# Optimization experiments

Measured on AMD Instinct MI355X. Metric: run time of the kernel, lower is better.

Reference implementation:

```python
import jax, jax.numpy as jnp
import numpy as np

N_KNN = 16
BN_EPS = 1e-5


def conv1d(x, w, b):
    # x: [B, Cin, N], w: [Cout, Cin], b: [Cout] (1x1 Conv1d)
    return jnp.einsum('oc,bcn->bon', w, x) + b[None, :, None]


def conv2d(x, w, b):
    # x: [B, Cin, N, K], w: [Cout, Cin], b: [Cout] (1x1 Conv2d)
    return jnp.einsum('oc,bcnk->bonk', w, x) + b[None, :, None, None]


def bn2d(x, gamma, beta, mean, var):
    # eval-mode BatchNorm2d over channel axis 1
    scale = (gamma / jnp.sqrt(var + BN_EPS))[None, :, None, None]
    return (x - mean[None, :, None, None]) * scale + beta[None, :, None, None]


def knn_idx(pos, k):
    # pos: [B, 3, N] -> idx: [B, N, K] of k nearest neighbors (incl. self)
    p = jnp.swapaxes(pos, 1, 2)  # [B, N, 3]
    sq = jnp.sum(p * p, axis=-1)  # [B, N]
    d2 = sq[:, :, None] - 2.0 * jnp.einsum('bnd,bmd->bnm', p, p) + sq[:, None, :]
    _, idx = jax.lax.top_k(-d2, k)
    return idx


def group(x, idx):
    # x: [B, C, N], idx: [B, N, K] -> [B, C, N, K] (grouping_operation)
    return jax.vmap(lambda xb, ib: xb[:, ib])(x, idx)


def setup_inputs() -> dict:
    key = jax.random.key(0)
    B, C_OBJ, C_Q, N, DIM, PH, AM = 4, 512, 512, 4096, 128, 64, 4
    ks = jax.random.split(key, 32)
    r = lambda i, sh, s=0.05: jax.random.normal(ks[i], sh, jnp.float32) * s
    inp = {
        'obj_feature': jax.random.normal(ks[0], (B, C_OBJ, N), jnp.float32),
        'pos': jax.random.normal(ks[1], (B, 3, N), jnp.float32),
        'query_points': jax.random.normal(ks[2], (B, C_Q, N), jnp.float32),
        # linear_start_query / linear_start_obj
        'w_sq': r(3, (DIM, C_Q)), 'b_sq': r(4, (DIM,)),
        'w_so': r(5, (DIM, C_OBJ)), 'b_so': r(6, (DIM,)),
        # key / query / value 1x1 convs
        'w_k': r(7, (DIM, DIM)), 'b_k': r(8, (DIM,)),
        'w_q': r(9, (DIM, DIM)), 'b_q': r(10, (DIM,)),
        'w_v': r(11, (DIM, DIM)), 'b_v': r(12, (DIM,)),
        # pos_mlp: Conv2d(3->PH), BN, ReLU, Conv2d(PH->DIM)
        'w_p1': r(13, (PH, 3)), 'b_p1': r(14, (PH,)),
        'g_bn1': 1.0 + r(15, (PH,)), 'be_bn1': r(16, (PH,)),
        'm_bn1': r(17, (PH,)), 'v_bn1': 1.0 + 0.1 * jax.random.uniform(ks[18], (PH,), jnp.float32),
        'w_p2': r(19, (DIM, PH)), 'b_p2': r(20, (DIM,)),
        # attn_mlp: Conv2d(DIM->DIM*AM), BN, ReLU, Conv2d(DIM*AM->DIM)
        'w_a1': r(21, (DIM * AM, DIM)), 'b_a1': r(22, (DIM * AM,)),
        'g_bn2': 1.0 + r(23, (DIM * AM,)), 'be_bn2': r(24, (DIM * AM,)),
        'm_bn2': r(25, (DIM * AM,)), 'v_bn2': 1.0 + 0.1 * jax.random.uniform(ks[26], (DIM * AM,), jnp.float32),
        # linear_end
        'w_e': r(27, (C_OBJ, DIM)), 'b_e': r(28, (C_OBJ,)),
    }
    return inp


def reference(obj_feature, pos, query_points, w_sq, b_sq, w_so, b_so, w_k, b_k,
              w_q, b_q, w_v, b_v, w_p1, b_p1, g_bn1, be_bn1, m_bn1, v_bn1,
              w_p2, b_p2, w_a1, b_a1, g_bn2, be_bn2, m_bn2, v_bn2, w_e, b_e):
    qf = conv1d(query_points, w_sq, b_sq)          # [B, dim, N]
    f = conv1d(obj_feature, w_so, b_so)            # [B, dim, N]
    idx = knn_idx(jax.lax.stop_gradient(pos), N_KNN)  # [B, N, K]
    key_g = group(conv1d(f, w_k, b_k), idx)        # [B, dim, N, K]
    value = conv1d(f, w_v, b_v)                    # [B, dim, N]
    query = conv1d(qf, w_q, b_q)                   # [B, dim, N]
    qk_rel = query[:, :, :, None] - key_g          # [B, dim, N, K]
    pos_rel = pos[:, :, :, None] - group(pos, idx)  # [B, 3, N, K]
    pe = conv2d(jax.nn.relu(bn2d(conv2d(pos_rel, w_p1, b_p1), g_bn1, be_bn1, m_bn1, v_bn1)), w_p2, b_p2)
    attn = conv2d(jax.nn.relu(bn2d(conv2d(qk_rel + pe, w_a1, b_a1), g_bn2, be_bn2, m_bn2, v_bn2)), w_a2_placeholder := w_p2 * 0 + 0, b_p2 * 0) if False else None
    hidden = jax.nn.relu(bn2d(conv2d(qk_rel + pe, w_a1, b_a1), g_bn2, be_bn2, m_bn2, v_bn2))
    attn = jax.nn.softmax(conv2d(hidden, w_a2, b_a2), axis=-1)  # softmax over K
    v = value[:, :, :, None] + pe                  # [B, dim, N, K]
    agg = jnp.sum(attn * v, axis=-1)               # 'b c i j, b c i j -> b c i'
    return conv1d(agg, w_e, b_e)                   # [B, C_obj, N]

# fix: w_a2/b_a2 are parameters; re-declare reference cleanly to include them

def _setup_extra(inp):
    kk = jax.random.split(jax.random.key(7), 2)
    inp['w_a2'] = jax.random.normal(kk[0], (128, 512), jnp.float32) * 0.05
    inp['b_a2'] = jax.random.normal(kk[1], (128,), jnp.float32) * 0.05
    return inp

_orig_setup = setup_inputs

def setup_inputs():
    return _setup_extra(_orig_setup())


def reference(obj_feature, pos, query_points, w_sq, b_sq, w_so, b_so, w_k, b_k,
              w_q, b_q, w_v, b_v, w_p1, b_p1, g_bn1, be_bn1, m_bn1, v_bn1,
              w_p2, b_p2, w_a1, b_a1, g_bn2, be_bn2, m_bn2, v_bn2, w_a2, b_a2,
              w_e, b_e):
    qf = conv1d(query_points, w_sq, b_sq)
    f = conv1d(obj_feature, w_so, b_so)
    idx = knn_idx(jax.lax.stop_gradient(pos), N_KNN)
    key_g = group(conv1d(f, w_k, b_k), idx)
    value = conv1d(f, w_v, b_v)
    query = conv1d(qf, w_q, b_q)
    qk_rel = query[:, :, :, None] - key_g
    pos_rel = pos[:, :, :, None] - group(pos, idx)
    pe = conv2d(jax.nn.relu(bn2d(conv2d(pos_rel, w_p1, b_p1), g_bn1, be_bn1, m_bn1, v_bn1)), w_p2, b_p2)
    hidden = jax.nn.relu(bn2d(conv2d(qk_rel + pe, w_a1, b_a1), g_bn2, be_bn2, m_bn2, v_bn2))
    attn = jax.nn.softmax(conv2d(hidden, w_a2, b_a2), axis=-1)
    v = value[:, :, :, None] + pe
    agg = jnp.sum(attn * v, axis=-1)
    return conv1d(agg, w_e, b_e)
```

## Files before the change

kernel.cpp:

```cpp
#include <hip/hip_runtime.h>

typedef __bf16 bf16;
typedef __bf16 bf16x8 __attribute__((ext_vector_type(8)));
typedef __bf16 bf16x4 __attribute__((ext_vector_type(4)));
typedef __bf16 bf16x2 __attribute__((ext_vector_type(2)));
typedef float f32x4 __attribute__((ext_vector_type(4)));

#define MFMA16(a,b,c) __builtin_amdgcn_mfma_f32_16x16x32_bf16((a),(b),(c),0,0,0)

#define NPTS 4096
#define CIN 512
#define DIM 128
#define PH 64
#define HID 512

#define OFF_WQS 0u
#define OFF_WKO (128u*1024u)
#define OFF_WVO (256u*1024u)
#define OFF_BQS (384u*1024u)
#define OFF_BKO (385u*1024u)
#define OFF_BVO (386u*1024u)
#define OFF_S1  (387u*1024u)
#define OFF_T1  (388u*1024u)
#define OFF_S2  (389u*1024u)
#define OFF_T2  (391u*1024u)
#define OFF_CW  (400u*1024u)
#define OFF_QT  (1u<<20)
#define OFF_KT  (OFF_QT + (4u<<20))
#define OFF_VT  (OFF_QT + (8u<<20))
#define OFF_IDX (OFF_QT + (12u<<20))
#define WS_NEED (OFF_QT + (13u<<20))

struct P {
  const float* in[31];
  char* ws;
  float* out;
};

template<int C> __device__ __forceinline__ float rorf(float x){
  return __int_as_float(__builtin_amdgcn_mov_dpp(__float_as_int(x), 0x120|C, 0xF, 0xF, true));
}
__device__ __forceinline__ float red16max(float x){
  x=fmaxf(x,rorf<1>(x)); x=fmaxf(x,rorf<2>(x)); x=fmaxf(x,rorf<4>(x)); x=fmaxf(x,rorf<8>(x)); return x;
}
__device__ __forceinline__ float red16sum(float x){
  x+=rorf<1>(x); x+=rorf<2>(x); x+=rorf<4>(x); x+=rorf<8>(x); return x;
}

__global__ __launch_bounds__(256) void k_fold(P p) {
  int tid = blockIdx.x*256 + threadIdx.x;
  char* ws = p.ws;
  if (tid < 196608) {
    int m_id = tid >> 16, o = (tid >> 9) & 127, c = tid & 511;
    const float* A  = m_id==0 ? p.in[9] : (m_id==1 ? p.in[7] : p.in[11]);
    const float* Bm = (m_id==0) ? p.in[3] : p.in[5];
    float acc = 0.f;
    #pragma unroll 8
    for (int m=0;m<128;m++) acc += A[o*128+m] * Bm[m*512+c];
    bf16* outw = (bf16*)(ws + (m_id==0?OFF_WQS: m_id==1?OFF_WKO:OFF_WVO));
    outw[o*512+c] = (bf16)acc;
  } else if (tid < 196992) {
    int t = tid - 196608; int m_id = t >> 7, o = t & 127;
    const float* A  = m_id==0 ? p.in[9] : (m_id==1 ? p.in[7] : p.in[11]);
    const float* bb = (m_id==0) ? p.in[4] : p.in[6];
    const float* bs = m_id==0 ? p.in[10] : (m_id==1 ? p.in[8] : p.in[12]);
    float acc = bs[o];
    for (int m=0;m<128;m++) acc += A[o*128+m] * bb[m];
    float* ob = (float*)(ws + (m_id==0?OFF_BQS: m_id==1?OFF_BKO:OFF_BVO));
    ob[o] = acc;
  } else if (tid < 197056) {
    int i = tid - 196992;
    float s = p.in[15][i] * rsqrtf(p.in[18][i] + 1e-5f);
    ((float*)(ws+OFF_S1))[i] = s;
    ((float*)(ws+OFF_T1))[i] = (p.in[14][i] - p.in[17][i])*s + p.in[16][i];
  } else if (tid < 197568) {
    int i = tid - 197056;
    float s = p.in[23][i] * rsqrtf(p.in[26][i] + 1e-5f);
    ((float*)(ws+OFF_S2))[i] = s;
    ((float*)(ws+OFF_T2))[i] = (p.in[22][i] - p.in[25][i])*s + p.in[24][i];
  } else if (tid < 223168) {
    int e0 = (tid - 197568) * 8;
    const float* src; int base;
    if (e0 < 8192)        { src = p.in[19]; base = 0; }
    else if (e0 < 73728)  { src = p.in[21]; base = 8192; }
    else if (e0 < 139264) { src = p.in[29]; base = 73728; }
    else                  { src = p.in[27]; base = 139264; }
    const float* sp = src + (e0 - base);
    f32x4 a = *(const f32x4*)sp, b2 = *(const f32x4*)(sp+4);
    bf16x8 o8;
    o8[0]=(bf16)a[0]; o8[1]=(bf16)a[1]; o8[2]=(bf16)a[2]; o8[3]=(bf16)a[3];
    o8[4]=(bf16)b2[0]; o8[5]=(bf16)b2[1]; o8[6]=(bf16)b2[2]; o8[7]=(bf16)b2[3];
    *(bf16x8*)((bf16*)(ws+OFF_CW) + e0) = o8;
  }
}

__global__ __launch_bounds__(256) void k_knn(P p) {
  int lane = threadIdx.x & 63, w = threadIdx.x >> 6;
  int ig = blockIdx.x*4 + w;
  int b = ig >> 12, n = ig & 4095;
  const float* pb = p.in[1] + b*3*NPTS;
  float qx = pb[n], qy = pb[NPTS+n], qz = pb[2*NPTS+n];
  float sqn = __fadd_rn(__fadd_rn(__fmul_rn(qx,qx), __fmul_rn(qy,qy)), __fmul_rn(qz,qz));
  unsigned u[64];
  #pragma unroll
  for (int t=0;t<64;t++) {
    int j = t*64 + lane;
    float xj=pb[j], yj=pb[NPTS+j], zj=pb[2*NPTS+j];
    float sqj = __fadd_rn(__fadd_rn(__fmul_rn(xj,xj), __fmul_rn(yj,yj)), __fmul_rn(zj,zj));
    float dot = __fadd_rn(__fadd_rn(__fmul_rn(qx,xj), __fmul_rn(qy,yj)), __fmul_rn(qz,zj));
    float d2 = __fadd_rn(__fsub_rn(sqn, __fmul_rn(2.f,dot)), sqj);
    unsigned bbits = __float_as_uint(d2);
    u[t] = bbits ^ (((unsigned)((int)bbits >> 31)) | 0x80000000u);
  }
  int* op = (int*)(p.ws + OFF_IDX) + ig*16;
  int tsel_s = 64; bool mine = false;
  #pragma unroll 1
  for (int r=0;r<16;r++) {
    switch (tsel_s) {
#define CLR(T) case T: u[T] = mine ? 0xFFFFFFFFu : u[T]; break;
      CLR(0) CLR(1) CLR(2) CLR(3) CLR(4) CLR(5) CLR(6) CLR(7)
      CLR(8) CLR(9) CLR(10) CLR(11) CLR(12) CLR(13) CLR(14) CLR(15)
      CLR(16) CLR(17) CLR(18) CLR(19) CLR(20) CLR(21) CLR(22) CLR(23)
      CLR(24) CLR(25) CLR(26) CLR(27) CLR(28) CLR(29) CLR(30) CLR(31)
      CLR(32) CLR(33) CLR(34) CLR(35) CLR(36) CLR(37) CLR(38) CLR(39)
      CLR(40) CLR(41) CLR(42) CLR(43) CLR(44) CLR(45) CLR(46) CLR(47)
      CLR(48) CLR(49) CLR(50) CLR(51) CLR(52) CLR(53) CLR(54) CLR(55)
      CLR(56) CLR(57) CLR(58) CLR(59) CLR(60) CLR(61) CLR(62) CLR(63)
#undef CLR
      default: break;
    }
    unsigned vmin = 0xFFFFFFFFu; int tmin = 0;
    #pragma unroll
    for (int t=0;t<64;t++) {
      bool lt = u[t] < vmin;
      vmin = lt ? u[t] : vmin;
      tmin = lt ? t : tmin;
    }
    int jmin = (tmin<<6) | lane;
    #pragma unroll
    for (int off=32; off>0; off>>=1) {
      unsigned vo = (unsigned)__shfl_xor((int)vmin, off);
      int jo = __shfl_xor(jmin, off);
      bool take = (vo < vmin) || (vo == vmin && (unsigned)jo < (unsigned)jmin);
      vmin = take ? vo : vmin;
      jmin = take ? jo : jmin;
    }
    if (lane==0) op[r] = jmin;
    tsel_s = __builtin_amdgcn_readfirstlane(jmin >> 6);
    mine = (lane == (jmin & 63));
  }
}

__global__ __launch_bounds__(256) void k_qkv(P p) {
  int mat = blockIdx.z, b = blockIdx.y, n0 = blockIdx.x*64;
  int tid = threadIdx.x, lane = tid&63, w = tid>>6;
  const float* in = (mat==0 ? p.in[2] : p.in[0]) + b*CIN*NPTS;
  const bf16* W = (const bf16*)(p.ws + (mat==0?OFF_WQS: mat==1?OFF_WKO:OFF_WVO));
  const float* bias = (const float*)(p.ws + (mat==0?OFF_BQS: mat==1?OFF_BKO:OFF_BVO));
  bf16* outT = (bf16*)(p.ws + (mat==0?OFF_QT: mat==1?OFF_KT:OFF_VT)) + (b*NPTS + n0)*DIM;
  __shared__ __align__(16) bf16 Bl[64*40];
  f32x4 acc[8] = {};
  for (int ks=0; ks<16; ks++) {
    int c0 = ks*32;
    {
      int cc = tid>>3, nn0 = (tid&7)*8;
      const float* sp = in + (c0+cc)*NPTS + n0 + nn0;
      f32x4 a = *(const f32x4*)sp, b2 = *(const f32x4*)(sp+4);
      Bl[(nn0+0)*40+cc]=(bf16)a[0];  Bl[(nn0+1)*40+cc]=(bf16)a[1];
      Bl[(nn0+2)*40+cc]=(bf16)a[2];  Bl[(nn0+3)*40+cc]=(bf16)a[3];
      Bl[(nn0+4)*40+cc]=(bf16)b2[0]; Bl[(nn0+5)*40+cc]=(bf16)b2[1];
      Bl[(nn0+6)*40+cc]=(bf16)b2[2]; Bl[(nn0+7)*40+cc]=(bf16)b2[3];
    }
    __syncthreads();
    int ncol = w*16 + (lane&15);
    bf16x8 bfr = *(const bf16x8*)(&Bl[ncol*40 + (lane>>4)*8]);
    #pragma unroll
    for (int ot=0;ot<8;ot++) {
      bf16x8 af = *(const bf16x8*)(W + (ot*16 + (lane&15))*CIN + c0 + (lane>>4)*8);
      acc[ot] = MFMA16(af, bfr, acc[ot]);
    }
    __syncthreads();
  }
  int o0 = (lane>>4)*4;
  int nloc = w*16 + (lane&15);
  #pragma unroll
  for (int ot=0;ot<8;ot++) {
    f32x4 bs = *(const f32x4*)(bias + ot*16 + o0);
    bf16x4 st;
    st[0]=(bf16)(acc[ot][0]+bs[0]); st[1]=(bf16)(acc[ot][1]+bs[1]);
    st[2]=(bf16)(acc[ot][2]+bs[2]); st[3]=(bf16)(acc[ot][3]+bs[3]);
    *(bf16x4*)(outT + nloc*DIM + ot*16 + o0) = st;
  }
}

__global__ __launch_bounds__(512) void k_fused(P p) {
  int bb = blockIdx.y, pt0 = blockIdx.x*8;
  int tid=threadIdx.x, lane=tid&63, w=tid>>6;
  int c = lane&15, g = lane>>4;
  char* ws = p.ws;
  const bf16* qT = (const bf16*)(ws+OFF_QT) + bb*NPTS*DIM;
  const bf16* kT = (const bf16*)(ws+OFF_KT) + bb*NPTS*DIM;
  const bf16* vT = (const bf16*)(ws+OFF_VT) + bb*NPTS*DIM;
  const int* idxg = (const int*)(ws+OFF_IDX) + (bb*NPTS + pt0)*16;
  const bf16* wp2b = (const bf16*)(ws+OFF_CW);
  const bf16* wa1b = wp2b + 8192;
  const bf16* wa2b = wa1b + 65536;
  const bf16* web  = wa2b + 65536;
  const float* s2 = (const float*)(ws+OFF_S2);
  const float* t2 = (const float*)(ws+OFF_T2);
  __shared__ __align__(16) bf16 Xl[128*136];
  __shared__ __align__(16) bf16 HT[128*136];
  __shared__ __align__(16) bf16 aggl[16*136];
  __shared__ float prl[128][4];
  __shared__ int idxl[128];

  if (tid < 128) {
    int j = idxg[tid] & 4095;
    idxl[tid] = j;
    const float* pb = p.in[1] + bb*3*NPTS;
    int n = pt0 + (tid>>4);
    prl[tid][0] = pb[n]        - pb[j];
    prl[tid][1] = pb[NPTS+n]   - pb[NPTS+j];
    prl[tid][2] = pb[2*NPTS+n] - pb[2*NPTS+j];
  } else if (tid >= 256 && tid < 392) {
    f32x4 z = {};
    *(f32x4*)((char*)aggl + 2176 + (tid-256)*16) = z;
  }
  __syncthreads();

  {
    int col = tid & 127, mb = (tid>>7)*16;
    float r0=prl[col][0], r1=prl[col][1], r2=prl[col][2];
    const float* wp1 = p.in[13];
    const float* s1 = (const float*)(ws+OFF_S1);
    const float* t1 = (const float*)(ws+OFF_T1);
    #pragma unroll
    for (int i=0;i<16;i+=2) {
      int m = mb+i;
      float x0 = wp1[m*3]*r0   + wp1[m*3+1]*r1 + wp1[m*3+2]*r2;
      float x1 = wp1[m*3+3]*r0 + wp1[m*3+4]*r1 + wp1[m*3+5]*r2;
      bf16x2 pk;
      pk[0] = (bf16)fmaxf(0.f, x0*s1[m]   + t1[m]);
      pk[1] = (bf16)fmaxf(0.f, x1*s1[m+1] + t1[m+1]);
      *(bf16x2*)(&HT[col*136 + m]) = pk;
    }
  }
  __syncthreads();

  {
    f32x4 acc[8] = {};
    int crow = w*16 + c;
    #pragma unroll
    for (int ksx=0; ksx<2; ksx++) {
      int m0 = ksx*32 + g*8;
      bf16x8 af = *(const bf16x8*)(wp2b + crow*PH + m0);
      #pragma unroll
      for (int nt=0; nt<8; nt++) {
        int col = nt*16 + c;
        bf16x8 bfr = *(const bf16x8*)(&HT[col*136 + m0]);
        acc[nt] = MFMA16(af, bfr, acc[nt]);
      }
    }
    int c0 = w*16 + g*4;
    f32x4 bp4 = *(const f32x4*)(p.in[20] + c0);
    #pragma unroll
    for (int nt=0; nt<8; nt++) {
      int col = nt*16 + c;
      int j = idxl[col];
      int n = pt0 + nt;
      bf16x4 q4 = *(const bf16x4*)(qT + n*DIM + c0);
      bf16x4 k4 = *(const bf16x4*)(kT + j*DIM + c0);
      bf16x4 st;
      #pragma unroll
      for (int r=0;r<4;r++)
        st[r] = (bf16)((float)q4[r] - (float)k4[r] + acc[nt][r] + bp4[r]);
      *(bf16x4*)(&Xl[col*136 + c0]) = st;
    }
  }
  __syncthreads();

  f32x4 S[2][4] = {{{},{},{},{}},{{},{},{},{}}};
  int h32 = (w&3)*32, ch64 = (w>>2)*64;
  #pragma unroll 1
  for (int cc4=0; cc4<4; cc4++) {
    int hbase = cc4*128;
    f32x4 acc[2][4] = {{{},{},{},{}},{{},{},{},{}}};
    #pragma unroll
    for (int ksx=0;ksx<4;ksx++) {
      int k0 = ksx*32 + g*8;
      bf16x8 af0 = *(const bf16x8*)(wa1b + (hbase+h32+c)*DIM + k0);
      bf16x8 af1 = *(const bf16x8*)(wa1b + (hbase+h32+16+c)*DIM + k0);
      #pragma unroll
      for (int cg=0;cg<4;cg++) {
        bf16x8 bfr = *(const bf16x8*)(&Xl[(ch64+cg*16+c)*136 + k0]);
        acc[0][cg] = MFMA16(af0, bfr, acc[0][cg]);
        acc[1][cg] = MFMA16(af1, bfr, acc[1][cg]);
      }
    }
    #pragma unroll
    for (int mt2=0;mt2<2;mt2++) {
      int hg = hbase + h32 + mt2*16 + g*4;
      f32x4 sv = *(const f32x4*)(s2+hg), tv = *(const f32x4*)(t2+hg);
      int hloc = h32 + mt2*16 + g*4;
      #pragma unroll
      for (int cg=0;cg<4;cg++) {
        int col = ch64+cg*16+c;
        bf16x4 st;
        st[0]=(bf16)fmaxf(0.f, acc[mt2][cg][0]*sv[0]+tv[0]);
        st[1]=(bf16)fmaxf(0.f, acc[mt2][cg][1]*sv[1]+tv[1]);
        st[2]=(bf16)fmaxf(0.f, acc[mt2][cg][2]*sv[2]+tv[2]);
        st[3]=(bf16)fmaxf(0.f, acc[mt2][cg][3]*sv[3]+tv[3]);
        *(bf16x4*)(&HT[col*136 + hloc]) = st;
      }
    }
    __syncthreads();
    #pragma unroll
    for (int ksx=0;ksx<4;ksx++) {
      int k0 = ksx*32 + g*8;
      bf16x8 af0 = *(const bf16x8*)(wa2b + (h32+c)*HID + hbase + k0);
      bf16x8 af1 = *(const bf16x8*)(wa2b + (h32+16+c)*HID + hbase + k0);
      #pragma unroll
      for (int cg=0;cg<4;cg++) {
        bf16x8 bfr = *(const bf16x8*)(&HT[(ch64+cg*16+c)*136 + k0]);
        S[0][cg] = MFMA16(af0, bfr, S[0][cg]);
        S[1][cg] = MFMA16(af1, bfr, S[1][cg]);
      }
    }
    __syncthreads();
  }

  #pragma unroll
  for (int mt2=0;mt2<2;mt2++) {
    #pragma unroll
    for (int cg=0;cg<4;cg++) {
      int ptl = (w>>2)*4 + cg;
      int pt = pt0 + ptl;
      int col = ch64 + cg*16 + c;
      int j = idxl[col];
      int chb = h32 + mt2*16 + g*4;
      bf16x4 x4 = *(const bf16x4*)(&Xl[col*136 + chb]);
      bf16x4 q4 = *(const bf16x4*)(qT + pt*DIM + chb);
      bf16x4 k4 = *(const bf16x4*)(kT + j*DIM + chb);
      bf16x4 v4 = *(const bf16x4*)(vT + pt*DIM + chb);
      float agv[4];
      #pragma unroll
      for (int r=0;r<4;r++) {
        float s = S[mt2][cg][r];
        float mx = red16max(s);
        float e = __expf(s-mx);
        float sm = red16sum(e);
        float at = e/sm;
        float vpe = (float)v4[r] + (float)x4[r] - (float)q4[r] + (float)k4[r];
        agv[r] = red16sum(at*vpe);
      }
      if (c==0) {
        bf16x4 st; st[0]=(bf16)agv[0]; st[1]=(bf16)agv[1]; st[2]=(bf16)agv[2]; st[3]=(bf16)agv[3];
        *(bf16x4*)(&aggl[ptl*136 + chb]) = st;
      }
    }
  }
  __syncthreads();

  {
    const float* be = p.in[28];
    f32x4 acc5[4] = {};
    #pragma unroll
    for (int ksx=0; ksx<4; ksx++) {
      int pcol = c;
      bf16x8 bfr = *(const bf16x8*)(&aggl[pcol*136 + ksx*32 + g*8]);
      #pragma unroll
      for (int i=0;i<4;i++) {
        int e = (w*4+i)*16 + c;
        bf16x8 af = *(const bf16x8*)(web + e*DIM + ksx*32 + g*8);
        acc5[i] = MFMA16(af, bfr, acc5[i]);
      }
    }
    if (c < 8) {
      int n = pt0 + c;
      #pragma unroll
      for (int i=0;i<4;i++) {
        int e0 = (w*4+i)*16 + g*4;
        f32x4 be4 = *(const f32x4*)(be + e0);
        #pragma unroll
        for (int r=0;r<4;r++)
          p.out[(bb*CIN + e0+r)*NPTS + n] = acc5[i][r] + be4[r];
      }
    }
  }
}

extern "C" void kernel_launch(void* const* d_in, const int* in_sizes, int n_in,
                              void* d_out, int out_size, void* d_ws, size_t ws_size,
                              hipStream_t stream) {
  if (ws_size < WS_NEED || n_in < 31) return;
  P p;
  for (int i=0;i<31;i++) p.in[i] = (const float*)d_in[i];
  p.ws = (char*)d_ws;
  p.out = (float*)d_out;
  k_fold<<<872, 256, 0, stream>>>(p);
  k_knn<<<4096, 256, 0, stream>>>(p);
  k_qkv<<<dim3(64, 4, 3), 256, 0, stream>>>(p);
  k_fused<<<dim3(512, 4), 512, 0, stream>>>(p);
}
```

Measured before the change: 483.3 us.

## Shrink fused-kernel LDS footprint and rechunk attention MLP hidden dimension

Packs the fused kernel's shared memory into one 52 KB buffer. The hidden tile now uses 64-wide chunks with stride 72, and the aggregate buffer aliases the hidden tile. The idx and pos-rel staging arrays are dropped in favour of direct global reads. The attention MLP is re-tiled into eight 64-row hidden chunks, with each wave owning 16 output channels across all 8 points. This makes the softmax and aggregation mapping match the earlier pe stage. The aim is to fit more blocks per CU by cutting LDS use, at the cost of twice as many barriers and the loss of zero-init for unused aggregate rows. The fused launch is also split into two half-batch launches.

```diff
diff --git a/kernel.cpp b/kernel.cpp
--- a/kernel.cpp
+++ b/kernel.cpp
@@ -35,6 +35,7 @@
   const float* in[31];
   char* ws;
   float* out;
+  int ybase;
 };
 
 template<int C> __device__ __forceinline__ float rorf(float x){
@@ -194,7 +195,7 @@
 }
 
 __global__ __launch_bounds__(512) void k_fused(P p) {
-  int bb = blockIdx.y, pt0 = blockIdx.x*8;
+  int bb = p.ybase + blockIdx.y, pt0 = blockIdx.x*8;
   int tid=threadIdx.x, lane=tid&63, w=tid>>6;
   int c = lane&15, g = lane>>4;
   char* ws = p.ws;
@@ -208,41 +209,29 @@
   const bf16* web  = wa2b + 65536;
   const float* s2 = (const float*)(ws+OFF_S2);
   const float* t2 = (const float*)(ws+OFF_T2);
-  __shared__ __align__(16) bf16 Xl[128*136];
-  __shared__ __align__(16) bf16 HT[128*136];
-  __shared__ __align__(16) bf16 aggl[16*136];
-  __shared__ float prl[128][4];
-  __shared__ int idxl[128];
-
-  if (tid < 128) {
-    int j = idxg[tid] & 4095;
-    idxl[tid] = j;
+  __shared__ __align__(16) char LB[53248];
+  bf16* Xl = (bf16*)LB;
+  bf16* HT = (bf16*)(LB + 34816);
+  bf16* aggl = (bf16*)(LB + 34816);
+
+  {
+    int col = w*16 + c;
+    int j = idxg[col] & 4095;
     const float* pb = p.in[1] + bb*3*NPTS;
-    int n = pt0 + (tid>>4);
-    prl[tid][0] = pb[n]        - pb[j];
-    prl[tid][1] = pb[NPTS+n]   - pb[NPTS+j];
-    prl[tid][2] = pb[2*NPTS+n] - pb[2*NPTS+j];
-  } else if (tid >= 256 && tid < 392) {
-    f32x4 z = {};
-    *(f32x4*)((char*)aggl + 2176 + (tid-256)*16) = z;
-  }
-  __syncthreads();
-
-  {
-    int col = tid & 127, mb = (tid>>7)*16;
-    float r0=prl[col][0], r1=prl[col][1], r2=prl[col][2];
+    int n = pt0 + w;
+    float r0 = pb[n]-pb[j], r1 = pb[NPTS+n]-pb[NPTS+j], r2 = pb[2*NPTS+n]-pb[2*NPTS+j];
     const float* wp1 = p.in[13];
     const float* s1 = (const float*)(ws+OFF_S1);
     const float* t1 = (const float*)(ws+OFF_T1);
     #pragma unroll
     for (int i=0;i<16;i+=2) {
-      int m = mb+i;
+      int m = g*16 + i;
       float x0 = wp1[m*3]*r0   + wp1[m*3+1]*r1 + wp1[m*3+2]*r2;
       float x1 = wp1[m*3+3]*r0 + wp1[m*3+4]*r1 + wp1[m*3+5]*r2;
       bf16x2 pk;
       pk[0] = (bf16)fmaxf(0.f, x0*s1[m]   + t1[m]);
       pk[1] = (bf16)fmaxf(0.f, x1*s1[m+1] + t1[m+1]);
-      *(bf16x2*)(&HT[col*136 + m]) = pk;
+      *(bf16x2*)(&HT[col*72 + m]) = pk;
     }
   }
   __syncthreads();
@@ -257,7 +246,7 @@
       #pragma unroll
       for (int nt=0; nt<8; nt++) {
         int col = nt*16 + c;
-        bf16x8 bfr = *(const bf16x8*)(&HT[col*136 + m0]);
+        bf16x8 bfr = *(const bf16x8*)(&HT[col*72 + m0]);
         acc[nt] = MFMA16(af, bfr, acc[nt]);
       }
     }
@@ -266,7 +255,7 @@
     #pragma unroll
     for (int nt=0; nt<8; nt++) {
       int col = nt*16 + c;
-      int j = idxl[col];
+      int j = idxg[col] & 4095;
       int n = pt0 + nt;
       bf16x4 q4 = *(const bf16x4*)(qT + n*DIM + c0);
       bf16x4 k4 = *(const bf16x4*)(kT + j*DIM + c0);
@@ -279,75 +268,67 @@
   }
   __syncthreads();
 
-  f32x4 S[2][4] = {{{},{},{},{}},{{},{},{},{}}};
-  int h32 = (w&3)*32, ch64 = (w>>2)*64;
-  #pragma unroll 1
-  for (int cc4=0; cc4<4; cc4++) {
-    int hbase = cc4*128;
-    f32x4 acc[2][4] = {{{},{},{},{}},{{},{},{},{}}};
-    #pragma unroll
-    for (int ksx=0;ksx<4;ksx++) {
-      int k0 = ksx*32 + g*8;
-      bf16x8 af0 = *(const bf16x8*)(wa1b + (hbase+h32+c)*DIM + k0);
-      bf16x8 af1 = *(const bf16x8*)(wa1b + (hbase+h32+16+c)*DIM + k0);
-      #pragma unroll
-      for (int cg=0;cg<4;cg++) {
-        bf16x8 bfr = *(const bf16x8*)(&Xl[(ch64+cg*16+c)*136 + k0]);
-        acc[0][cg] = MFMA16(af0, bfr, acc[0][cg]);
-        acc[1][cg] = MFMA16(af1, bfr, acc[1][cg]);
-      }
-    }
-    #pragma unroll
-    for (int mt2=0;mt2<2;mt2++) {
-      int hg = hbase + h32 + mt2*16 + g*4;
-      f32x4 sv = *(const f32x4*)(s2+hg), tv = *(const f32x4*)(t2+hg);
-      int hloc = h32 + mt2*16 + g*4;
-      #pragma unroll
-      for (int cg=0;cg<4;cg++) {
-        int col = ch64+cg*16+c;
-        bf16x4 st;
-        st[0]=(bf16)fmaxf(0.f, acc[mt2][cg][0]*sv[0]+tv[0]);
-        st[1]=(bf16)fmaxf(0.f, acc[mt2][cg][1]*sv[1]+tv[1]);
-        st[2]=(bf16)fmaxf(0.f, acc[mt2][cg][2]*sv[2]+tv[2]);
-        st[3]=(bf16)fmaxf(0.f, acc[mt2][cg][3]*sv[3]+tv[3]);
-        *(bf16x4*)(&HT[col*136 + hloc]) = st;
-      }
+  f32x4 S[8] = {};
+  for (int ch=0; ch<8; ch++) {
+    f32x4 acc1[4] = {};
+    int mtw = w & 3, nbase = (w>>2)*4;
+    int hrow = ch*64 + mtw*16 + c;
+    #pragma unroll
+    for (int ksx=0; ksx<4; ksx++) {
+      bf16x8 af = *(const bf16x8*)(wa1b + hrow*DIM + ksx*32 + g*8);
+      #pragma unroll
+      for (int i=0; i<4; i++) {
+        int col = (nbase+i)*16 + c;
+        bf16x8 bfr = *(const bf16x8*)(&Xl[col*136 + ksx*32 + g*8]);
+        acc1[i] = MFMA16(af, bfr, acc1[i]);
+      }
+    }
+    int h0 = ch*64 + mtw*16 + g*4;
+    int h0loc = mtw*16 + g*4;
+    f32x4 sv = *(const f32x4*)(s2 + h0);
+    f32x4 tv = *(const f32x4*)(t2 + h0);
+    #pragma unroll
+    for (int i=0;i<4;i++) {
+      int col = (nbase+i)*16 + c;
+      bf16x4 st;
+      st[0]=(bf16)fmaxf(0.f, acc1[i][0]*sv[0]+tv[0]);
+      st[1]=(bf16)fmaxf(0.f, acc1[i][1]*sv[1]+tv[1]);
+      st[2]=(bf16)fmaxf(0.f, acc1[i][2]*sv[2]+tv[2]);
+      st[3]=(bf16)fmaxf(0.f, acc1[i][3]*sv[3]+tv[3]);
+      *(bf16x4*)(&HT[col*72 + h0loc]) = st;
     }
     __syncthreads();
-    #pragma unroll
-    for (int ksx=0;ksx<4;ksx++) {
-      int k0 = ksx*32 + g*8;
-      bf16x8 af0 = *(const bf16x8*)(wa2b + (h32+c)*HID + hbase + k0);
-      bf16x8 af1 = *(const bf16x8*)(wa2b + (h32+16+c)*HID + hbase + k0);
-      #pragma unroll
-      for (int cg=0;cg<4;cg++) {
-        bf16x8 bfr = *(const bf16x8*)(&HT[(ch64+cg*16+c)*136 + k0]);
-        S[0][cg] = MFMA16(af0, bfr, S[0][cg]);
-        S[1][cg] = MFMA16(af1, bfr, S[1][cg]);
+    int orow = w*16 + c;
+    #pragma unroll
+    for (int ksx=0; ksx<2; ksx++) {
+      bf16x8 af = *(const bf16x8*)(wa2b + orow*HID + ch*64 + ksx*32 + g*8);
+      #pragma unroll
+      for (int nt=0; nt<8; nt++) {
+        int col = nt*16 + c;
+        bf16x8 bfr = *(const bf16x8*)(&HT[col*72 + ksx*32 + g*8]);
+        S[nt] = MFMA16(af, bfr, S[nt]);
       }
     }
     __syncthreads();
   }
 
-  #pragma unroll
-  for (int mt2=0;mt2<2;mt2++) {
-    #pragma unroll
-    for (int cg=0;cg<4;cg++) {
-      int ptl = (w>>2)*4 + cg;
-      int pt = pt0 + ptl;
-      int col = ch64 + cg*16 + c;
-      int j = idxl[col];
-      int chb = h32 + mt2*16 + g*4;
-      bf16x4 x4 = *(const bf16x4*)(&Xl[col*136 + chb]);
-      bf16x4 q4 = *(const bf16x4*)(qT + pt*DIM + chb);
-      bf16x4 k4 = *(const bf16x4*)(kT + j*DIM + chb);
-      bf16x4 v4 = *(const bf16x4*)(vT + pt*DIM + chb);
+  {
+    int c0 = w*16 + g*4;
+    #pragma unroll
+    for (int nt=0; nt<8; nt++) {
+      f32x4 s = S[nt];
+      int col = nt*16 + c;
+      int j = idxg[col] & 4095;
+      int n = pt0 + nt;
+      bf16x4 x4 = *(const bf16x4*)(&Xl[col*136 + c0]);
+      bf16x4 q4 = *(const bf16x4*)(qT + n*DIM + c0);
+      bf16x4 k4 = *(const bf16x4*)(kT + j*DIM + c0);
+      bf16x4 v4 = *(const bf16x4*)(vT + n*DIM + c0);
       float agv[4];
       #pragma unroll
       for (int r=0;r<4;r++) {
-        float s = S[mt2][cg][r];
-        float mx = red16max(s);
-        float e = __expf(s-mx);
+        float mx = red16max(s[r]);
+        float e = __expf(s[r]-mx);
         float sm = red16sum(e);
         float at = e/sm;
         float vpe = (float)v4[r] + (float)x4[r] - (float)q4[r] + (float)k4[r];
@@ -355,7 +336,7 @@
       }
       if (c==0) {
         bf16x4 st; st[0]=(bf16)agv[0]; st[1]=(bf16)agv[1]; st[2]=(bf16)agv[2]; st[3]=(bf16)agv[3];
-        *(bf16x4*)(&aggl[ptl*136 + chb]) = st;
+        *(bf16x4*)(&aggl[nt*136 + c0]) = st;
       }
     }
   }
@@ -366,8 +347,7 @@
     f32x4 acc5[4] = {};
     #pragma unroll
     for (int ksx=0; ksx<4; ksx++) {
-      int pcol = c;
-      bf16x8 bfr = *(const bf16x8*)(&aggl[pcol*136 + ksx*32 + g*8]);
+      bf16x8 bfr = *(const bf16x8*)(&aggl[c*136 + ksx*32 + g*8]);
       #pragma unroll
       for (int i=0;i<4;i++) {
         int e = (w*4+i)*16 + c;
@@ -397,8 +377,11 @@
   for (int i=0;i<31;i++) p.in[i] = (const float*)d_in[i];
   p.ws = (char*)d_ws;
   p.out = (float*)d_out;
+  p.ybase = 0;
   k_fold<<<872, 256, 0, stream>>>(p);
   k_knn<<<4096, 256, 0, stream>>>(p);
   k_qkv<<<dim3(64, 4, 3), 256, 0, stream>>>(p);
-  k_fused<<<dim3(512, 4), 512, 0, stream>>>(p);
-}
+  k_fused<<<dim3(512, 2), 512, 0, stream>>>(p);
+  P p2 = p; p2.ybase = 2;
+  k_fused<<<dim3(512, 2), 512, 0, stream>>>(p2);
+}
```

Result: faster. 467.9 us (-3.2%).
